# Performance work log

Hardware: AMD Instinct MI355X
Metric: run time of the kernel (lower is better)

The kernel has to match this reference:

```python
import jax, jax.numpy as jnp
import numpy as np

FP8_MAX = 448.0  # max finite value of float8_e4m3fn

def _quant_fp8(v):
    # round to fp8_e4m3fn grid, keep values in fp32 (simulates fp8 storage)
    return v.astype(jnp.float8_e4m3fn).astype(jnp.float32)

def setup_inputs() -> dict:
    key = jax.random.key(0)
    k1, k2, k3 = jax.random.split(key, 3)
    M, K, N = 4096, 4096, 16384  # tokens, input_size, output_size
    x = jax.random.normal(k1, (M, K), dtype=jnp.float32)
    # build a per-output-channel (per_Token quant of the weight) fp8 weight
    w = jax.random.normal(k2, (N, K), dtype=jnp.float32) * 0.02
    weight_scale = jnp.max(jnp.abs(w), axis=1, keepdims=True) / FP8_MAX  # [N,1] fp32
    weight = _quant_fp8(w / weight_scale)  # fp8 codes stored as fp32
    bias = jax.random.normal(k3, (N,), dtype=jnp.float32) * 0.01
    return {"x": x, "weight": weight, "weight_scale": weight_scale, "bias": bias}

def reference(x, weight, weight_scale, bias):
    # --- dynamic per-token quantization of the activations (x_scale is None path) ---
    x_scale = jnp.max(jnp.abs(x), axis=-1, keepdims=True) / FP8_MAX  # [M,1]
    x_scale = jnp.maximum(x_scale, 1e-12)
    xq = _quant_fp8(x / x_scale)  # fp8 activation codes
    # --- a8w8 GEMM with fp32 accumulation, fused dequant + bias ---
    y = jnp.einsum('mk,nk->mn', xq, weight)          # [M,N] fp32 accum
    y = y * x_scale * weight_scale.T + bias          # per-token * per-channel dequant
    return y
```

## Files before the change

kernel.cpp:

```cpp
#include <hip/hip_runtime.h>

#define M_DIM 4096
#define K_DIM 4096
#define N_DIM 16384

typedef float v4f __attribute__((ext_vector_type(4)));

__global__ __launch_bounds__(256) void quant_x_kernel(
    const float* __restrict__ x, unsigned char* __restrict__ xq,
    float* __restrict__ xs) {
  const int row = blockIdx.x;
  const int t = threadIdx.x;
  const float4* xr4 = (const float4*)(x + (size_t)row * K_DIM);

  float4 v[4];
  float am = 0.f;
#pragma unroll
  for (int i = 0; i < 4; ++i) {
    v[i] = xr4[t + 256 * i];
    am = fmaxf(am, fmaxf(fmaxf(fabsf(v[i].x), fabsf(v[i].y)),
                         fmaxf(fabsf(v[i].z), fabsf(v[i].w))));
  }
#pragma unroll
  for (int off = 32; off > 0; off >>= 1)
    am = fmaxf(am, __shfl_xor(am, off, 64));
  __shared__ float red[4];
  if ((t & 63) == 0) red[t >> 6] = am;
  __syncthreads();
  am = fmaxf(fmaxf(red[0], red[1]), fmaxf(red[2], red[3]));

  const float scale = fmaxf(am / 448.0f, 1e-12f);
  if (t == 0) xs[row] = scale;

  uint32_t* out = (uint32_t*)(xq + (size_t)row * K_DIM);
#pragma unroll
  for (int i = 0; i < 4; ++i) {
    float a0 = v[i].x / scale, a1 = v[i].y / scale;
    float a2 = v[i].z / scale, a3 = v[i].w / scale;
    uint32_t p = __builtin_amdgcn_cvt_pk_fp8_f32(a0, a1, 0, false);
    p = __builtin_amdgcn_cvt_pk_fp8_f32(a2, a3, p, true);
    out[t + 256 * i] = p;
  }
}

__global__ __launch_bounds__(256) void quant_w_kernel(
    const float4* __restrict__ w, uint32_t* __restrict__ wq) {
  const int i = blockIdx.x * 256 + threadIdx.x;
  float4 v = w[i];
  uint32_t p = __builtin_amdgcn_cvt_pk_fp8_f32(v.x, v.y, 0, false);
  p = __builtin_amdgcn_cvt_pk_fp8_f32(v.z, v.w, p, true);
  wq[i] = p;
}

__device__ __forceinline__ void async_copy16(const void* g, void* l) {
  __builtin_amdgcn_global_load_lds(
      (const __attribute__((address_space(1))) void*)g,
      (__attribute__((address_space(3))) void*)l, 16, 0, 0);
}

__global__ __launch_bounds__(256) void gemm_fp8_kernel(
    const unsigned char* __restrict__ Aq,
    const unsigned char* __restrict__ Bq,
    const float* __restrict__ xs,
    const float* __restrict__ wscale,
    const float* __restrict__ bias,
    float* __restrict__ y) {
  constexpr int BM = 128, BN = 128, BK = 64;
  __shared__ __align__(16) unsigned char smem[(BM + BN) * BK];
  unsigned char* sA = smem;
  unsigned char* sB = smem + BM * BK;

  const int t = threadIdx.x;
  const int bm = blockIdx.y * BM;
  const int bn = blockIdx.x * BN;

  const int srow = t >> 2;
  const int scol = (((t & 3) ^ ((srow >> 1) & 3)) * 16);
  const unsigned char* Ag0 = Aq + (size_t)(bm + srow) * K_DIM + scol;
  const unsigned char* Ag1 = Aq + (size_t)(bm + srow + 64) * K_DIM + scol;
  const unsigned char* Bg0 = Bq + (size_t)(bn + srow) * K_DIM + scol;
  const unsigned char* Bg1 = Bq + (size_t)(bn + srow + 64) * K_DIM + scol;

  const int lane = t & 63;
  const int w = t >> 6;
  const int wm = (w >> 1) * 64;
  const int wn = (w & 1) * 64;
  const int lrow = lane & 15;
  const int lq = lane >> 4;
  const int xm = ((lrow >> 1) & 3) << 4;

  v4f acc[4][4];
#pragma unroll
  for (int i = 0; i < 4; ++i)
#pragma unroll
    for (int j = 0; j < 4; ++j) acc[i][j] = {0.f, 0.f, 0.f, 0.f};

  for (int k0 = 0; k0 < K_DIM; k0 += BK) {
    __syncthreads();
    async_copy16(Ag0 + k0, sA + t * 16);
    async_copy16(Ag1 + k0, sA + (t + 256) * 16);
    async_copy16(Bg0 + k0, sB + t * 16);
    async_copy16(Bg1 + k0, sB + (t + 256) * 16);
    __syncthreads();

#pragma unroll
    for (int kk = 0; kk < BK; kk += 32) {
      const int koff = (kk + lq * 8) ^ xm;
      long long a_frag[4], b_frag[4];
#pragma unroll
      for (int i = 0; i < 4; ++i)
        a_frag[i] = *(const long long*)(sA + (wm + i * 16 + lrow) * BK + koff);
#pragma unroll
      for (int j = 0; j < 4; ++j)
        b_frag[j] = *(const long long*)(sB + (wn + j * 16 + lrow) * BK + koff);
#pragma unroll
      for (int i = 0; i < 4; ++i)
#pragma unroll
        for (int j = 0; j < 4; ++j)
          acc[i][j] = __builtin_amdgcn_mfma_f32_16x16x32_fp8_fp8(
              a_frag[i], b_frag[j], acc[i][j], 0, 0, 0);
    }
  }

  float xsv[4][4];
#pragma unroll
  for (int i = 0; i < 4; ++i)
#pragma unroll
    for (int r = 0; r < 4; ++r)
      xsv[i][r] = xs[bm + wm + i * 16 + lq * 4 + r];

#pragma unroll
  for (int j = 0; j < 4; ++j) {
    const int col = bn + wn + j * 16 + lrow;
    const float wsc = wscale[col];
    const float bv = bias[col];
#pragma unroll
    for (int i = 0; i < 4; ++i) {
      const int row0 = bm + wm + i * 16 + lq * 4;
#pragma unroll
      for (int r = 0; r < 4; ++r)
        y[(size_t)(row0 + r) * N_DIM + col] =
            acc[i][j][r] * xsv[i][r] * wsc + bv;
    }
  }
}

extern "C" void kernel_launch(void* const* d_in, const int* in_sizes, int n_in,
                              void* d_out, int out_size, void* d_ws,
                              size_t ws_size, hipStream_t stream) {
  const float* x = (const float*)d_in[0];
  const float* w = (const float*)d_in[1];
  const float* wscale = (const float*)d_in[2];
  const float* bias = (const float*)d_in[3];
  float* y = (float*)d_out;

  unsigned char* xq = (unsigned char*)d_ws;
  unsigned char* wq = xq + (size_t)M_DIM * K_DIM;
  float* xs = (float*)(wq + (size_t)N_DIM * K_DIM);

  quant_x_kernel<<<M_DIM, 256, 0, stream>>>(x, xq, xs);
  quant_w_kernel<<<((size_t)N_DIM * K_DIM / 4) / 256, 256, 0, stream>>>(
      (const float4*)w, (uint32_t*)wq);
  dim3 grid(N_DIM / 128, M_DIM / 128);
  gemm_fp8_kernel<<<grid, 256, 0, stream>>>(xq, wq, xs, wscale, bias, y);
}
```

Measured before the change: 984.3 us.

## Rewrite FP8 GEMM with 256x256 tiles, triple-buffered async LDS pipeline

The GEMM kernel moves from 128x128 tiles with 256 threads to 256x256 tiles with 512 threads. It uses a three-stage LDS ring buffer fed by async global-to-LDS copies, with explicit vmcnt/lgkmcnt waits and barriers so loads for later K-steps overlap MFMA work. It also adds a swizzled 1D block-to-tile mapping for L2 locality, s_setprio around MFMA bursts, and hand-scheduled ds_read_b64 fragments. In exchange it uses 96KB of LDS and more accumulator registers per thread, which limits occupancy, and it relies on fragile manual waitcnt ordering.

```diff
diff --git a/kernel.cpp b/kernel.cpp
--- a/kernel.cpp
+++ b/kernel.cpp
@@ -5,6 +5,7 @@
 #define N_DIM 16384
 
 typedef float v4f __attribute__((ext_vector_type(4)));
+typedef __attribute__((address_space(3))) unsigned char lds_uchar;
 
 __global__ __launch_bounds__(256) void quant_x_kernel(
     const float* __restrict__ x, unsigned char* __restrict__ xq,
@@ -58,85 +59,167 @@
       (__attribute__((address_space(3))) void*)l, 16, 0, 0);
 }
 
-__global__ __launch_bounds__(256) void gemm_fp8_kernel(
+__device__ __forceinline__ long long lds_read_b64(const lds_uchar* p) {
+  long long d;
+  asm volatile("ds_read_b64 %0, %1" : "=v"(d) : "v"(p));
+  return d;
+}
+
+#define MF(a, b, c) __builtin_amdgcn_mfma_f32_16x16x32_fp8_fp8(a, b, c, 0, 0, 0)
+
+#define AOFF(i, ks) ((ks) ? (aoff[i] ^ 32u) : aoff[i])
+#define BOFF(j, ks) ((ks) ? (boff[j] ^ 32u) : boff[j])
+
+#define PHASE(ks, mh, STAGE_STMT, TAIL_STMT)                            \
+  {                                                                     \
+    fa0 = lds_read_b64(bb + AOFF(4 * (mh) + 0, ks));                    \
+    fa1 = lds_read_b64(bb + AOFF(4 * (mh) + 1, ks));                    \
+    fa2 = lds_read_b64(bb + AOFF(4 * (mh) + 2, ks));                    \
+    fa3 = lds_read_b64(bb + AOFF(4 * (mh) + 3, ks));                    \
+    if ((mh) == 0) {                                                    \
+      fb0 = lds_read_b64(bb + BOFF(0, ks));                             \
+      fb1 = lds_read_b64(bb + BOFF(1, ks));                             \
+      fb2 = lds_read_b64(bb + BOFF(2, ks));                             \
+      fb3 = lds_read_b64(bb + BOFF(3, ks));                             \
+    }                                                                   \
+    STAGE_STMT;                                                         \
+    __builtin_amdgcn_s_barrier();                                       \
+    asm volatile("s_waitcnt lgkmcnt(0)");                               \
+    __builtin_amdgcn_sched_barrier(0);                                  \
+    __builtin_amdgcn_s_setprio(1);                                      \
+    acc[4 * (mh) + 0][0] = MF(fa0, fb0, acc[4 * (mh) + 0][0]);          \
+    acc[4 * (mh) + 0][1] = MF(fa0, fb1, acc[4 * (mh) + 0][1]);          \
+    acc[4 * (mh) + 0][2] = MF(fa0, fb2, acc[4 * (mh) + 0][2]);          \
+    acc[4 * (mh) + 0][3] = MF(fa0, fb3, acc[4 * (mh) + 0][3]);          \
+    acc[4 * (mh) + 1][0] = MF(fa1, fb0, acc[4 * (mh) + 1][0]);          \
+    acc[4 * (mh) + 1][1] = MF(fa1, fb1, acc[4 * (mh) + 1][1]);          \
+    acc[4 * (mh) + 1][2] = MF(fa1, fb2, acc[4 * (mh) + 1][2]);          \
+    acc[4 * (mh) + 1][3] = MF(fa1, fb3, acc[4 * (mh) + 1][3]);          \
+    acc[4 * (mh) + 2][0] = MF(fa2, fb0, acc[4 * (mh) + 2][0]);          \
+    acc[4 * (mh) + 2][1] = MF(fa2, fb1, acc[4 * (mh) + 2][1]);          \
+    acc[4 * (mh) + 2][2] = MF(fa2, fb2, acc[4 * (mh) + 2][2]);          \
+    acc[4 * (mh) + 2][3] = MF(fa2, fb3, acc[4 * (mh) + 2][3]);          \
+    acc[4 * (mh) + 3][0] = MF(fa3, fb0, acc[4 * (mh) + 3][0]);          \
+    acc[4 * (mh) + 3][1] = MF(fa3, fb1, acc[4 * (mh) + 3][1]);          \
+    acc[4 * (mh) + 3][2] = MF(fa3, fb2, acc[4 * (mh) + 3][2]);          \
+    acc[4 * (mh) + 3][3] = MF(fa3, fb3, acc[4 * (mh) + 3][3]);          \
+    __builtin_amdgcn_sched_barrier(0);                                  \
+    __builtin_amdgcn_s_setprio(0);                                      \
+    TAIL_STMT;                                                          \
+    __builtin_amdgcn_s_barrier();                                       \
+  }
+
+#define TILE(DO_STAGE, TAIL_STMT)                                       \
+  PHASE(0, 0, if (DO_STAGE) async_copy16(gA0 + kst, sd), (void)0)       \
+  PHASE(0, 1, if (DO_STAGE) async_copy16(gA1 + kst, sd + 8192), (void)0)\
+  PHASE(1, 0, if (DO_STAGE) async_copy16(gB0 + kst, sd + 16384), (void)0)\
+  PHASE(1, 1, if (DO_STAGE) async_copy16(gB1 + kst, sd + 24576), TAIL_STMT)
+
+__global__ __launch_bounds__(512, 2) void gemm_fp8_kernel(
     const unsigned char* __restrict__ Aq,
     const unsigned char* __restrict__ Bq,
     const float* __restrict__ xs,
     const float* __restrict__ wscale,
     const float* __restrict__ bias,
     float* __restrict__ y) {
-  constexpr int BM = 128, BN = 128, BK = 64;
-  __shared__ __align__(16) unsigned char smem[(BM + BN) * BK];
-  unsigned char* sA = smem;
-  unsigned char* sB = smem + BM * BK;
-
-  const int t = threadIdx.x;
-  const int bm = blockIdx.y * BM;
-  const int bn = blockIdx.x * BN;
-
-  const int srow = t >> 2;
-  const int scol = (((t & 3) ^ ((srow >> 1) & 3)) * 16);
-  const unsigned char* Ag0 = Aq + (size_t)(bm + srow) * K_DIM + scol;
-  const unsigned char* Ag1 = Aq + (size_t)(bm + srow + 64) * K_DIM + scol;
-  const unsigned char* Bg0 = Bq + (size_t)(bn + srow) * K_DIM + scol;
-  const unsigned char* Bg1 = Bq + (size_t)(bn + srow + 64) * K_DIM + scol;
-
-  const int lane = t & 63;
-  const int w = t >> 6;
-  const int wm = (w >> 1) * 64;
-  const int wn = (w & 1) * 64;
+  constexpr int BK = 64;
+  __shared__ __align__(16) unsigned char smem[3 * 32768];
+
+  const int tid = threadIdx.x;
+
+  const int id = blockIdx.x;
+  const int sw = (id & 7) * 128 + (id >> 3);
+  const int bm = (sw >> 6) * 256;
+  const int bn = (sw & 63) * 256;
+
+  const int srow = tid >> 2;
+  const unsigned scol = (unsigned)(((tid & 3) ^ ((srow >> 1) & 3)) * 16);
+  const unsigned char* gA0 = Aq + (size_t)(bm + srow) * K_DIM + scol;
+  const unsigned char* gA1 = gA0 + (size_t)128 * K_DIM;
+  const unsigned char* gB0 = Bq + (size_t)(bn + srow) * K_DIM + scol;
+  const unsigned char* gB1 = gB0 + (size_t)128 * K_DIM;
+
+  const int lane = tid & 63;
+  const int w = tid >> 6;
+  const int wmo = (w >> 2) * 128;
+  const int wno = (w & 3) * 64;
   const int lrow = lane & 15;
   const int lq = lane >> 4;
-  const int xm = ((lrow >> 1) & 3) << 4;
-
-  v4f acc[4][4];
-#pragma unroll
-  for (int i = 0; i < 4; ++i)
+  const unsigned xm = (unsigned)(((lrow >> 1) & 3) << 4);
+  const unsigned koff0 = ((unsigned)(lq * 8)) ^ xm;
+
+  unsigned aoff[8], boff[4];
+#pragma unroll
+  for (int i = 0; i < 8; ++i)
+    aoff[i] = (unsigned)((wmo + i * 16 + lrow) * 64) + koff0;
+#pragma unroll
+  for (int j = 0; j < 4; ++j)
+    boff[j] = 16384u + (unsigned)((wno + j * 16 + lrow) * 64) + koff0;
+
+  v4f acc[8][4];
+#pragma unroll
+  for (int i = 0; i < 8; ++i)
 #pragma unroll
     for (int j = 0; j < 4; ++j) acc[i][j] = {0.f, 0.f, 0.f, 0.f};
 
-  for (int k0 = 0; k0 < K_DIM; k0 += BK) {
-    __syncthreads();
-    async_copy16(Ag0 + k0, sA + t * 16);
-    async_copy16(Ag1 + k0, sA + (t + 256) * 16);
-    async_copy16(Bg0 + k0, sB + t * 16);
-    async_copy16(Bg1 + k0, sB + (t + 256) * 16);
-    __syncthreads();
-
-#pragma unroll
-    for (int kk = 0; kk < BK; kk += 32) {
-      const int koff = (kk + lq * 8) ^ xm;
-      long long a_frag[4], b_frag[4];
-#pragma unroll
-      for (int i = 0; i < 4; ++i)
-        a_frag[i] = *(const long long*)(sA + (wm + i * 16 + lrow) * BK + koff);
-#pragma unroll
-      for (int j = 0; j < 4; ++j)
-        b_frag[j] = *(const long long*)(sB + (wn + j * 16 + lrow) * BK + koff);
-#pragma unroll
-      for (int i = 0; i < 4; ++i)
-#pragma unroll
-        for (int j = 0; j < 4; ++j)
-          acc[i][j] = __builtin_amdgcn_mfma_f32_16x16x32_fp8_fp8(
-              a_frag[i], b_frag[j], acc[i][j], 0, 0, 0);
-    }
-  }
-
-  float xsv[4][4];
-#pragma unroll
-  for (int i = 0; i < 4; ++i)
+  long long fa0, fa1, fa2, fa3;
+  long long fb0 = 0, fb1 = 0, fb2 = 0, fb3 = 0;
+
+  {
+    unsigned char* s0 = smem + tid * 16;
+    async_copy16(gA0, s0);
+    async_copy16(gA1, s0 + 8192);
+    async_copy16(gB0, s0 + 16384);
+    async_copy16(gB1, s0 + 24576);
+    unsigned char* s1 = s0 + 32768;
+    async_copy16(gA0 + BK, s1);
+    async_copy16(gA1 + BK, s1 + 8192);
+    async_copy16(gB0 + BK, s1 + 16384);
+    async_copy16(gB1 + BK, s1 + 24576);
+  }
+  asm volatile("s_waitcnt vmcnt(4)");
+  __builtin_amdgcn_s_barrier();
+
+  int cur = 0, stg = 2;
+  for (int t = 0; t < 62; ++t) {
+    const lds_uchar* bb = (const lds_uchar*)(smem + cur * 32768);
+    unsigned char* sd = smem + stg * 32768 + tid * 16;
+    const int kst = (t + 2) * BK;
+    TILE(1, asm volatile("s_waitcnt vmcnt(4)"))
+    cur = (cur == 2) ? 0 : cur + 1;
+    stg = (stg == 2) ? 0 : stg + 1;
+  }
+  {
+    const lds_uchar* bb = (const lds_uchar*)(smem + cur * 32768);
+    unsigned char* sd = smem + tid * 16;
+    const int kst = 0;
+    TILE(0, asm volatile("s_waitcnt vmcnt(0)"))
+    cur = (cur == 2) ? 0 : cur + 1;
+  }
+  {
+    const lds_uchar* bb = (const lds_uchar*)(smem + cur * 32768);
+    unsigned char* sd = smem + tid * 16;
+    const int kst = 0;
+    TILE(0, (void)0)
+  }
+
+  const int bmw = bm + wmo;
+  const int bnw = bn + wno;
+  float xsv[8][4];
+#pragma unroll
+  for (int i = 0; i < 8; ++i)
 #pragma unroll
     for (int r = 0; r < 4; ++r)
-      xsv[i][r] = xs[bm + wm + i * 16 + lq * 4 + r];
+      xsv[i][r] = xs[bmw + i * 16 + lq * 4 + r];
 
 #pragma unroll
   for (int j = 0; j < 4; ++j) {
-    const int col = bn + wn + j * 16 + lrow;
+    const int col = bnw + j * 16 + lrow;
     const float wsc = wscale[col];
     const float bv = bias[col];
 #pragma unroll
-    for (int i = 0; i < 4; ++i) {
-      const int row0 = bm + wm + i * 16 + lq * 4;
+    for (int i = 0; i < 8; ++i) {
+      const int row0 = bmw + i * 16 + lq * 4;
 #pragma unroll
       for (int r = 0; r < 4; ++r)
         y[(size_t)(row0 + r) * N_DIM + col] =
@@ -161,6 +244,6 @@
   quant_x_kernel<<<M_DIM, 256, 0, stream>>>(x, xq, xs);
   quant_w_kernel<<<((size_t)N_DIM * K_DIM / 4) / 256, 256, 0, stream>>>(
       (const float4*)w, (uint32_t*)wq);
-  dim3 grid(N_DIM / 128, M_DIM / 128);
-  gemm_fp8_kernel<<<grid, 256, 0, stream>>>(xq, wq, xs, wscale, bias, y);
-}
+  gemm_fp8_kernel<<<(M_DIM / 256) * (N_DIM / 256), 512, 0, stream>>>(
+      xq, wq, xs, wscale, bias, y);
+}
```

Measured after the change: 842.3 us. -14.4%, faster.
